# Kernel tuning notes

Hardware: AMD Instinct MI355X
Metric: run time of the kernel (lower is better)

## Reference

```python
import jax, jax.numpy as jnp
import numpy as np

DEPTH, HEADS, DH, BUCKET, NHASH = 4, 8, 64, 64, 4
DIM, VOCAB, BATCH, SEQ = 512, 50000, 2, 2048
LN_EPS = 1e-5
SELF_ATTN_VAL = -5e4  # TOKEN_SELF_ATTN_VALUE in reformer_pytorch


def layer_norm(x, s, b):
    mu = x.mean(-1, keepdims=True)
    var = ((x - mu) ** 2).mean(-1, keepdims=True)
    return (x - mu) / jnp.sqrt(var + LN_EPS) * s + b


def sincos(t, dh):
    # FixedPositionalEmbedding: emb = cat(sin, cos) of t x dh/2 angles
    inv = 1.0 / (10000.0 ** (jnp.arange(0, dh, 2, dtype=jnp.float32) / dh))
    ang = jnp.arange(t, dtype=jnp.float32)[:, None] * inv[None, :]
    return jnp.sin(ang), jnp.cos(ang)


def apply_rotary(qk, sin, cos):
    # qk: [B*H, T, DH]; sin/cos: [T, DH/2]; interleaved-pair rotary as in reformer_pytorch
    sin2 = jnp.repeat(sin, 2, axis=-1)[None]
    cos2 = jnp.repeat(cos, 2, axis=-1)[None]
    xr = qk.reshape(qk.shape[0], qk.shape[1], -1, 2)
    rot = jnp.stack((-xr[..., 1], xr[..., 0]), axis=-1).reshape(qk.shape)
    return qk * cos2 + rot * sin2


def lsh_attention(qk, v, rot):
    # qk, v: [B, T, dh] (B = batch*heads, shared-QK); rot: [dh, NHASH, n_buckets//2]
    B, T, dh = qk.shape
    nb = T // BUCKET
    rv = jnp.einsum('btf,fhi->bhti', qk, rot)           # [B, NHASH, T, nb/2]
    rv = jnp.concatenate([rv, -rv], axis=-1)
    buckets = jnp.argmax(rv, axis=-1)                    # [B, NHASH, T]
    buckets = (buckets + (jnp.arange(NHASH) * nb)[None, :, None]).reshape(B, NHASH * T)
    ticker = jnp.arange(NHASH * T) % T
    key = T * buckets + ticker[None, :]                  # unique sort keys
    sticker = jnp.argsort(key, axis=-1)                  # [B, NHASH*T]
    undo = jnp.argsort(sticker, axis=-1)
    st = sticker % T
    sqk = jnp.take_along_axis(qk, st[:, :, None], axis=1)
    sv = jnp.take_along_axis(v, st[:, :, None], axis=1)
    C = NHASH * nb                                       # num chunks, each BUCKET long
    bq_t = st.reshape(B, C, BUCKET)
    bq = sqk.reshape(B, C, BUCKET, dh)
    bv = sv.reshape(B, C, BUCKET, dh)
    bk = bq / jnp.maximum(jnp.linalg.norm(bq, axis=-1, keepdims=True), 1e-12)

    def look_one_back(a):
        return jnp.concatenate([a, jnp.roll(a, 1, axis=1)], axis=2)

    bk, bv, bkv_t = look_one_back(bk), look_one_back(bv), look_one_back(bq_t)
    dots = jnp.einsum('bcie,bcje->bcij', bq, bk) * (dh ** -0.5)
    dots = jnp.where(bq_t[:, :, :, None] == bkv_t[:, :, None, :], SELF_ATTN_VAL, dots)
    lse = jax.nn.logsumexp(dots, axis=-1, keepdims=True)
    p = jnp.exp(dots - lse)
    bo = jnp.einsum('bcij,bcje->bcie', p, bv)
    so = bo.reshape(B, NHASH * T, dh)
    slog = lse.reshape(B, NHASH * T)
    o = jnp.take_along_axis(so, undo[:, :, None], axis=1).reshape(B, NHASH, T, dh)
    lg = jnp.take_along_axis(slog, undo, axis=1).reshape(B, NHASH, T, 1)
    w = jnp.exp(lg - jax.nn.logsumexp(lg, axis=1, keepdims=True))
    return jnp.sum(o * w, axis=1)                        # [B, T, dh]


def attn_block(x, s, bln, Wqk, Wv, Wo, bo, rot, sin, cos):
    b, t, _ = x.shape
    xn = layer_norm(x, s, bln)
    qk = (xn @ Wqk).reshape(b, t, HEADS, DH).transpose(0, 2, 1, 3).reshape(b * HEADS, t, DH)
    v = (xn @ Wv).reshape(b, t, HEADS, DH).transpose(0, 2, 1, 3).reshape(b * HEADS, t, DH)
    qk = apply_rotary(qk, sin, cos)
    o = lsh_attention(qk, v, rot)
    o = o.reshape(b, HEADS, t, DH).transpose(0, 2, 1, 3).reshape(b, t, HEADS * DH)
    return o @ Wo + bo


def ff_block(x, s, b, W1, b1, W2, b2):
    xn = layer_norm(x, s, b)
    return jax.nn.gelu(xn @ W1 + b1, approximate=False) @ W2 + b2


def reference(x, token_emb, ln1_s, ln1_b, Wqk, Wv, Wo, bo, ln2_s, ln2_b, W1, b1, W2, b2, rotations, lnf_s, lnf_b, Wf1, bf1, Wout, bout):
    e = token_emb[x]                                     # [B, T, DIM]
    sin, cos = sincos(x.shape[1], DH)
    x1 = x2 = e                                          # reversible twin streams
    for i in range(DEPTH):
        x1 = x1 + attn_block(x2, ln1_s[i], ln1_b[i], Wqk[i], Wv[i], Wo[i], bo[i], rotations[i], sin, cos)
        x2 = x2 + ff_block(x1, ln2_s[i], ln2_b[i], W1[i], b1[i], W2[i], b2[i])
    h = layer_norm((x1 + x2) * 0.5, lnf_s, lnf_b)
    h = h.mean(axis=1)
    h = jax.nn.relu(h @ Wf1 + bf1)
    return h @ Wout + bout


def setup_inputs():
    key = jax.random.key(0)
    ks = jax.random.split(key, 10)
    nb = SEQ // BUCKET
    s = 0.02
    return {
        'x': jax.random.randint(ks[0], (BATCH, SEQ), 0, VOCAB),
        'token_emb': jax.random.normal(ks[1], (VOCAB, DIM), jnp.float32) * s,
        'ln1_s': jnp.ones((DEPTH, DIM), jnp.float32),
        'ln1_b': jnp.zeros((DEPTH, DIM), jnp.float32),
        'Wqk': jax.random.normal(ks[2], (DEPTH, DIM, HEADS * DH), jnp.float32) * s,
        'Wv': jax.random.normal(ks[3], (DEPTH, DIM, HEADS * DH), jnp.float32) * s,
        'Wo': jax.random.normal(ks[4], (DEPTH, HEADS * DH, DIM), jnp.float32) * s,
        'bo': jnp.zeros((DEPTH, DIM), jnp.float32),
        'ln2_s': jnp.ones((DEPTH, DIM), jnp.float32),
        'ln2_b': jnp.zeros((DEPTH, DIM), jnp.float32),
        'W1': jax.random.normal(ks[5], (DEPTH, DIM, 4 * DIM), jnp.float32) * s,
        'b1': jnp.zeros((DEPTH, 4 * DIM), jnp.float32),
        'W2': jax.random.normal(ks[6], (DEPTH, 4 * DIM, DIM), jnp.float32) * s,
        'b2': jnp.zeros((DEPTH, DIM), jnp.float32),
        'rotations': jax.random.normal(ks[7], (DEPTH, DH, NHASH, nb // 2), jnp.float32),
        'lnf_s': jnp.ones((DIM,), jnp.float32),
        'lnf_b': jnp.zeros((DIM,), jnp.float32),
        'Wf1': jax.random.normal(ks[8], (DIM, 256), jnp.float32) * s,
        'bf1': jnp.zeros((256,), jnp.float32),
        'Wout': jax.random.normal(ks[9], (256, 1), jnp.float32) * s,
        'bout': jnp.zeros((1,), jnp.float32),
    }
```

## Files before the change

### kernel.cpp

```cpp
#include <hip/hip_runtime.h>
#include <math.h>

#define TSEQ   2048
#define DIMM   512
#define NHEAD  8
#define DHD    64
#define BHD    16
#define NHASHK 4
#define CHUNKS 128
#define FFD    2048
#define NROWS  4096

#define OFF_WQK 0
#define OFF_WV  262144
#define OFF_WO  524288
#define OFF_W1  786432
#define OFF_W2  1835008
#define WT_TOT  2883584

typedef unsigned short u16;
typedef _Float16 f16;
typedef __attribute__((ext_vector_type(8))) _Float16 f16x8;
typedef __attribute__((ext_vector_type(4))) float f32x4;
typedef __attribute__((ext_vector_type(8))) unsigned short ushort8v;
typedef __attribute__((ext_vector_type(4))) unsigned short ushort4v;

__device__ inline u16 h16(float f) {
  union { f16 h; u16 u; } x;
  x.h = (f16)f;
  return x.u;
}
__device__ inline float f16f(u16 u) {
  union { u16 u; f16 h; } x;
  x.u = u;
  return (float)x.h;
}
__device__ inline f16x8 mk8f(unsigned a, unsigned b, unsigned c, unsigned d) {
  union { unsigned u[4]; f16x8 v; } x;
  x.u[0] = a; x.u[1] = b; x.u[2] = c; x.u[3] = d;
  return x.v;
}
__device__ inline float gelu_exact(float v) {
  return 0.5f * v * (1.0f + erff(v * 0.70710678118654752f));
}
__device__ inline int swz128(int row, int colbyte) {
  return row * 128 + (colbyte ^ ((row & 7) << 4));
}
#define VT(d, k) ((d) * 264 + (((d) & 32) ? 8 : 0) + ((k) << 1))

__global__ __launch_bounds__(128) void k_embed(const int* __restrict__ x, const float* __restrict__ emb,
                                               float* __restrict__ x1, float* __restrict__ x2) {
  int row = blockIdx.x;
  int tok = x[row];
  float4 v = ((const float4*)(emb + (size_t)tok * DIMM))[threadIdx.x];
  ((float4*)(x1 + (size_t)row * DIMM))[threadIdx.x] = v;
  ((float4*)(x2 + (size_t)row * DIMM))[threadIdx.x] = v;
}

__global__ __launch_bounds__(256) void k_sincos(float* __restrict__ sin_t, float* __restrict__ cos_t) {
  int idx = blockIdx.x * 256 + threadIdx.x;
  int t = idx >> 5, i = idx & 31;
  float inv = powf(10000.0f, -(float)(2 * i) / 64.0f);
  float ang = (float)t * inv;
  sin_t[idx] = sinf(ang);
  cos_t[idx] = cosf(ang);
}

__global__ __launch_bounds__(256) void k_layernorm(const float* __restrict__ x, const float* __restrict__ g,
                                                   const float* __restrict__ b, u16* __restrict__ dst) {
  int row = blockIdx.x, tid = threadIdx.x;
  const float* xr = x + (size_t)row * DIMM;
  float v0 = xr[tid], v1 = xr[tid + 256];
  int lane = tid & 63, w = tid >> 6;
  __shared__ float red[8];
  float s = v0 + v1;
#pragma unroll
  for (int o = 32; o; o >>= 1) s += __shfl_xor(s, o);
  if (lane == 0) red[w] = s;
  __syncthreads();
  float mu = (red[0] + red[1] + red[2] + red[3]) * (1.0f / DIMM);
  float d0 = v0 - mu, d1 = v1 - mu;
  float q = d0 * d0 + d1 * d1;
#pragma unroll
  for (int o = 32; o; o >>= 1) q += __shfl_xor(q, o);
  if (lane == 0) red[4 + w] = q;
  __syncthreads();
  float var = (red[4] + red[5] + red[6] + red[7]) * (1.0f / DIMM);
  float rstd = 1.0f / sqrtf(var + 1e-5f);
  size_t base = (size_t)row * DIMM;
  dst[base + tid] = h16(d0 * rstd * g[tid] + b[tid]);
  dst[base + tid + 256] = h16(d1 * rstd * g[tid + 256] + b[tid + 256]);
}

__global__ __launch_bounds__(256) void k_prep(const float* __restrict__ Wqk, const float* __restrict__ Wv,
                                              const float* __restrict__ Wo, const float* __restrict__ W1,
                                              const float* __restrict__ W2, const float* __restrict__ rot,
                                              u16* __restrict__ wt16, u16* __restrict__ rt16) {
  __shared__ float tile[32][33];
  const int L = blockIdx.x / 2820;
  const int idx = blockIdx.x - L * 2820;
  Wqk += (size_t)L * 262144;
  Wv  += (size_t)L * 262144;
  Wo  += (size_t)L * 262144;
  W1  += (size_t)L * 1048576;
  W2  += (size_t)L * 1048576;
  rot += (size_t)L * 4096;
  u16* wt = wt16 + (size_t)L * WT_TOT;
  u16* rt = rt16 + (size_t)L * 4096;
  const float* src;
  u16* dh;
  int K, N, k0, n0;
  if (idx < 768) {
    int w = idx >> 8, r = idx & 255;
    K = 512; N = 512; k0 = (r >> 4) << 5; n0 = (r & 15) << 5;
    src = (w == 0) ? Wqk : (w == 1) ? Wv : Wo;
    dh = wt + (size_t)w * 262144;
  } else if (idx < 1792) {
    int r = idx - 768;
    K = 512; N = 2048; k0 = (r >> 6) << 5; n0 = (r & 63) << 5;
    src = W1; dh = wt + OFF_W1;
  } else if (idx < 2816) {
    int r = idx - 1792;
    K = 2048; N = 512; k0 = (r >> 4) << 5; n0 = (r & 15) << 5;
    src = W2; dh = wt + OFF_W2;
  } else {
    int r = idx - 2816;
    K = 64; N = 64; k0 = (r >> 1) << 5; n0 = (r & 1) << 5;
    src = rot; dh = rt;
  }
  const int t = threadIdx.x;
  const int r = t >> 3, c4 = (t & 7) << 2;
  float4 v = *(const float4*)&src[(size_t)(k0 + r) * N + n0 + c4];
  tile[r][c4] = v.x; tile[r][c4 + 1] = v.y; tile[r][c4 + 2] = v.z; tile[r][c4 + 3] = v.w;
  __syncthreads();
  u16 hs[4];
#pragma unroll
  for (int i = 0; i < 4; ++i) hs[i] = h16(tile[c4 + i][r]);
  size_t o = (size_t)(n0 + r) * K + k0 + c4;
  *(ushort4v*)&dh[o] = (ushort4v){hs[0], hs[1], hs[2], hs[3]};
}

template <int BM, int STORE>
__global__ __launch_bounds__(256) void k_gemm16(
    const u16* __restrict__ A, const u16* __restrict__ Bt,
    const float* __restrict__ bias, float* __restrict__ out,
    u16* __restrict__ out16, u16* __restrict__ qk16, u16* __restrict__ v16,
    int K, int N,
    const float* __restrict__ sin_t, const float* __restrict__ cos_t,
    const u16* __restrict__ rt16, int* __restrict__ bucket) {
  constexpr int MF = BM / 32;
  constexpr int ACH = BM / 32;
  __shared__ __align__(16) char AsB[BM * 128];
  __shared__ __align__(16) char BsB[64 * 128];
  const int bm = blockIdx.x * BM, bn = blockIdx.y << 6;
  const int tid = threadIdx.x, lane = tid & 63, wid = tid >> 6;
  const int wm = (wid >> 1) * (BM / 2), wn = (wid & 1) << 5;
  const int l16 = lane & 15, g = lane >> 4;
  f32x4 acc[MF][2];
#pragma unroll
  for (int m = 0; m < MF; ++m) { acc[m][0] = (f32x4){0,0,0,0}; acc[m][1] = (f32x4){0,0,0,0}; }

  const int srow = tid >> 3;
  const int scolb = (tid & 7) << 4;
  const u16* ap = A + (size_t)(bm + srow) * K + ((tid & 7) << 3);
  const u16* bp = Bt + (size_t)(bn + srow) * K + ((tid & 7) << 3);

  ushort8v paA[ACH], pbA[2], paB[ACH], pbB[2];
#pragma unroll
  for (int i = 0; i < ACH; ++i) paA[i] = *(const ushort8v*)(ap + (size_t)(i << 5) * K);
#pragma unroll
  for (int i = 0; i < 2; ++i) pbA[i] = *(const ushort8v*)(bp + (size_t)(i << 5) * K);
#pragma unroll
  for (int i = 0; i < ACH; ++i) paB[i] = *(const ushort8v*)(ap + (size_t)(i << 5) * K + 64);
#pragma unroll
  for (int i = 0; i < 2; ++i) pbB[i] = *(const ushort8v*)(bp + (size_t)(i << 5) * K + 64);

  auto gstep = [&](ushort8v (&PA)[ACH], ushort8v (&PB)[2], int S) {
#pragma unroll
    for (int i = 0; i < ACH; ++i)
      *(ushort8v*)(AsB + swz128(srow + (i << 5), scolb)) = PA[i];
#pragma unroll
    for (int i = 0; i < 2; ++i)
      *(ushort8v*)(BsB + swz128(srow + (i << 5), scolb)) = PB[i];
    __syncthreads();
    const int kf = (S + 2) << 6;
    if (kf < K) {
#pragma unroll
      for (int i = 0; i < ACH; ++i) PA[i] = *(const ushort8v*)(ap + (size_t)(i << 5) * K + kf);
#pragma unroll
      for (int i = 0; i < 2; ++i) PB[i] = *(const ushort8v*)(bp + (size_t)(i << 5) * K + kf);
    }
    f16x8 af[MF][2], bfr[2][2];
#pragma unroll
    for (int m = 0; m < MF; ++m)
#pragma unroll
      for (int ks = 0; ks < 2; ++ks)
        af[m][ks] = *(const f16x8*)(AsB + swz128(wm + (m << 4) + l16, ((ks << 2) + g) << 4));
#pragma unroll
    for (int n = 0; n < 2; ++n)
#pragma unroll
      for (int ks = 0; ks < 2; ++ks)
        bfr[n][ks] = *(const f16x8*)(BsB + swz128(wn + (n << 4) + l16, ((ks << 2) + g) << 4));
#pragma unroll
    for (int m = 0; m < MF; ++m)
#pragma unroll
      for (int n = 0; n < 2; ++n)
#pragma unroll
        for (int ks = 0; ks < 2; ++ks)
          acc[m][n] = __builtin_amdgcn_mfma_f32_16x16x32_f16(af[m][ks], bfr[n][ks], acc[m][n], 0, 0, 0);
    __syncthreads();
  };

  const int nsteps = K >> 6;
  for (int s = 0; s < nsteps; s += 2) {
    gstep(paA, pbA, s);
    gstep(paB, pbB, s + 1);
  }

  const bool do_bucket = (STORE == 5) && (bn < 512);
  ushort8v prt0{}, prt1{};
  if (do_bucket) {
    int i0 = tid, i1 = tid + 256;
    prt0 = *(const ushort8v*)(rt16 + (i0 >> 3) * 64 + ((i0 & 7) << 3));
    prt1 = *(const ushort8v*)(rt16 + (i1 >> 3) * 64 + ((i1 & 7) << 3));
  }

#pragma unroll
  for (int m = 0; m < MF; ++m) {
#pragma unroll
    for (int n = 0; n < 2; ++n) {
      const int gn = bn + wn + (n << 4) + l16;
      float bv = 0.f;
      if (STORE == 1 || STORE == 4) bv = bias[gn];
#pragma unroll
      for (int r = 0; r < 4; ++r) {
        const int gm = bm + wm + (m << 4) + (g << 2) + r;
        float val = acc[m][n][r];
        if (STORE == 1) {
          out[(size_t)gm * N + gn] += val + bv;
        } else if (STORE == 4) {
          out16[(size_t)gm * N + gn] = h16(gelu_exact(val + bv));
        } else {
          const float pv = __shfl_xor(val, 1);
          const int bb = gm >> 11, tt = gm & (TSEQ - 1);
          if (gn < 512) {
            const int hh = gn >> 6, dd = gn & 63;
            const int ip = dd >> 1;
            float cz = cos_t[tt * 32 + ip], sz = sin_t[tt * 32 + ip];
            float o = (dd & 1) ? (val * cz + pv * sz) : (val * cz - pv * sz);
            u16 oh = h16(o);
            qk16[((size_t)((bb * NHEAD + hh) * TSEQ + tt)) * DHD + dd] = oh;
            *(u16*)(AsB + swz128(gm - bm, dd << 1)) = oh;
          } else {
            const int gnn = gn - 512;
            const int hh = gnn >> 6, dd = gnn & 63;
            v16[((size_t)((bb * NHEAD + hh) * TSEQ + tt)) * DHD + dd] = h16(val);
          }
        }
      }
    }
  }

  if (do_bucket) {
    {
      int i0 = tid, i1 = tid + 256;
      *(ushort8v*)(BsB + swz128(i0 >> 3, (i0 & 7) << 4)) = prt0;
      *(ushort8v*)(BsB + swz128(i1 >> 3, (i1 & 7) << 4)) = prt1;
    }
    __syncthreads();
    const int bwm = (wid >> 1) << 5;
    const int bwn = (wid & 1) << 5;
    f32x4 bacc[2][2];
#pragma unroll
    for (int m = 0; m < 2; ++m) { bacc[m][0] = (f32x4){0,0,0,0}; bacc[m][1] = (f32x4){0,0,0,0}; }
#pragma unroll
    for (int ks = 0; ks < 2; ++ks) {
      f16x8 bfr[2];
#pragma unroll
      for (int n = 0; n < 2; ++n)
        bfr[n] = *(const f16x8*)(BsB + swz128(bwn + (n << 4) + l16, (ks << 6) + (g << 4)));
#pragma unroll
      for (int m = 0; m < 2; ++m) {
        f16x8 afr = *(const f16x8*)(AsB + swz128(bwm + (m << 4) + l16, (ks << 6) + (g << 4)));
#pragma unroll
        for (int n = 0; n < 2; ++n)
          bacc[m][n] = __builtin_amdgcn_mfma_f32_16x16x32_f16(afr, bfr[n], bacc[m][n], 0, 0, 0);
      }
    }
    const int bb = bm >> 11;
    const int hh = bn >> 6;
#pragma unroll
    for (int m = 0; m < 2; ++m)
#pragma unroll
      for (int n = 0; n < 2; ++n) {
        const int hcol = (bwn >> 4) + n;
#pragma unroll
        for (int r = 0; r < 4; ++r) {
          float v = bacc[m][n][r];
          float best = v; int bi = l16;
          if (-v > best) { best = -v; bi = 16 + l16; }
#pragma unroll
          for (int o = 1; o < 16; o <<= 1) {
            float ob = __shfl_xor(best, o);
            int obi = __shfl_xor(bi, o);
            if (ob > best || (ob == best && obi < bi)) { best = ob; bi = obi; }
          }
          if (l16 == 0) {
            int t = (bm & (TSEQ - 1)) + bwm + (m << 4) + (g << 2) + r;
            bucket[((size_t)((bb * NHEAD + hh) * NHASHK) + hcol) * TSEQ + t] = bi;
          }
        }
      }
  }
}

__global__ __launch_bounds__(256) void k_sort(const int* __restrict__ bucket, int* __restrict__ st) {
  __shared__ int hist[256][33];
  __shared__ int chunk[8][32];
  __shared__ int bbase[32];
  const int seg = blockIdx.x;
  const int tid = threadIdx.x;
  const int* bk = bucket + (size_t)seg * TSEQ;
  int4 u0 = *(const int4*)(bk + tid * 8);
  int4 u1 = *(const int4*)(bk + tid * 8 + 4);
  int myb[8] = {u0.x, u0.y, u0.z, u0.w, u1.x, u1.y, u1.z, u1.w};
#pragma unroll
  for (int j = 0; j < 33; ++j) hist[tid][j] = 0;
  __syncthreads();
#pragma unroll
  for (int i = 0; i < 8; ++i) hist[tid][myb[i]]++;
  __syncthreads();
  const int b = tid & 31, c = tid >> 5;
  int ssum = 0;
  for (int g2 = c * 32; g2 < c * 32 + 32; ++g2) ssum += hist[g2][b];
  chunk[c][b] = ssum;
  __syncthreads();
  if (tid < 32) {
    int run = 0;
    for (int cc = 0; cc < 8; ++cc) { int v = chunk[cc][tid]; chunk[cc][tid] = run; run += v; }
    bbase[tid] = run;
  }
  __syncthreads();
  if (tid == 0) {
    int s = 0;
    for (int j = 0; j < 32; ++j) { int v = bbase[j]; bbase[j] = s; s += v; }
  }
  __syncthreads();
  int run = chunk[c][b];
  for (int g2 = c * 32; g2 < c * 32 + 32; ++g2) { int v = hist[g2][b]; hist[g2][b] = run; run += v; }
  __syncthreads();
  int* dst = st + (size_t)seg * TSEQ;
#pragma unroll
  for (int i = 0; i < 8; ++i) {
    int bb2 = myb[i];
    int p = bbase[bb2] + hist[tid][bb2];
    hist[tid][bb2]++;
    dst[p] = tid * 8 + i;
  }
}

__global__ __launch_bounds__(256) void k_attn(const u16* __restrict__ qk16,
                                              const u16* __restrict__ v16,
                                              const int* __restrict__ st,
                                              u16* __restrict__ o4h, float* __restrict__ lg) {
  __shared__ __align__(16) char Kb[128 * 128];
  __shared__ __align__(16) char Vb[64 * 264 + 16];
  __shared__ float inv_norm[128];
  __shared__ int tids[128];
  __shared__ float pn[256];
  const int blk = blockIdx.x;
  const int c = blk & (CHUNKS - 1), bh = blk >> 7;
  const int h = c >> 5;
  const int tid = threadIdx.x, lane = tid & 63, wid = tid >> 6;
  const int l16 = lane & 15, g = lane >> 4;

  if (tid < 128) {
    int cc = (tid < 64) ? c : ((c + CHUNKS - 1) & (CHUNKS - 1));
    tids[tid] = st[bh * (NHASHK * TSEQ) + cc * 64 + (tid & 63)];
  }
  __syncthreads();
  {
    const int r = tid >> 1, hf = tid & 1;
    const u16* qsrc = qk16 + ((size_t)bh * TSEQ + tids[r]) * 64 + hf * 32;
    const u16* vsrc = v16 + ((size_t)bh * TSEQ + tids[r]) * 64 + hf * 32;
    float ss = 0.f;
#pragma unroll
    for (int i = 0; i < 4; ++i) {
      ushort8v u = *(const ushort8v*)(qsrc + i * 8);
      *(ushort8v*)(Kb + swz128(r, hf * 64 + i * 16)) = u;
#pragma unroll
      for (int j = 0; j < 8; ++j) { float f = f16f(u[j]); ss += f * f; }
      ushort8v vv8 = *(const ushort8v*)(vsrc + i * 8);
#pragma unroll
      for (int j = 0; j < 8; ++j)
        *(u16*)(Vb + VT(hf * 32 + i * 8 + j, r)) = vv8[j];
    }
    pn[tid] = ss;
  }
  __syncthreads();
  if (tid < 128) {
    float s2 = pn[2 * tid] + pn[2 * tid + 1];
    inv_norm[tid] = 1.0f / fmaxf(sqrtf(s2), 1e-12f);
  }
  __syncthreads();

  const int qrow = (wid << 4) + l16;
  const int tq = tids[qrow];
  const size_t obase = (size_t)(bh * NHASHK + h) * TSEQ + tq;

  f32x4 accs[8];
#pragma unroll
  for (int i = 0; i < 8; ++i) accs[i] = (f32x4){0, 0, 0, 0};
#pragma unroll
  for (int s = 0; s < 2; ++s) {
    f16x8 qf = *(const f16x8*)(Kb + swz128(qrow, ((s << 2) + g) << 4));
#pragma unroll
    for (int mf = 0; mf < 8; ++mf) {
      f16x8 afr = *(const f16x8*)(Kb + swz128(mf * 16 + l16, ((s << 2) + g) << 4));
      accs[mf] = __builtin_amdgcn_mfma_f32_16x16x32_f16(afr, qf, accs[mf], 0, 0, 0);
    }
  }
  float pv[8][4];
  float mx = -3e38f;
#pragma unroll
  for (int mf = 0; mf < 8; ++mf) {
    float4 invn = *(const float4*)&inv_norm[mf * 16 + g * 4];
    int4 tk = *(const int4*)&tids[mf * 16 + g * 4];
    float inva[4] = {invn.x, invn.y, invn.z, invn.w};
    int tka[4] = {tk.x, tk.y, tk.z, tk.w};
#pragma unroll
    for (int r = 0; r < 4; ++r) {
      float d = accs[mf][r] * inva[r] * 0.125f;
      if (tka[r] == tq) d = -5e4f;
      pv[mf][r] = d;
      mx = fmaxf(mx, d);
    }
  }
  mx = fmaxf(mx, __shfl_xor(mx, 16));
  mx = fmaxf(mx, __shfl_xor(mx, 32));
  float sum = 0.f;
#pragma unroll
  for (int mf = 0; mf < 8; ++mf)
#pragma unroll
    for (int r = 0; r < 4; ++r) {
      float e = __expf(pv[mf][r] - mx);
      pv[mf][r] = e;
      sum += e;
    }
  sum += __shfl_xor(sum, 16);
  sum += __shfl_xor(sum, 32);
  float lse = __logf(sum) + mx;
  float rs = 1.0f / sum;
  if (g == 0) lg[obase] = lse;
  unsigned P2[8][2];
#pragma unroll
  for (int mf = 0; mf < 8; ++mf)
#pragma unroll
    for (int m = 0; m < 2; ++m) {
      float p0 = pv[mf][2 * m] * rs, p1 = pv[mf][2 * m + 1] * rs;
      P2[mf][m] = (unsigned)h16(p0) | ((unsigned)h16(p1) << 16);
    }
  f32x4 acco[4];
#pragma unroll
  for (int i = 0; i < 4; ++i) acco[i] = (f32x4){0, 0, 0, 0};
#pragma unroll
  for (int s = 0; s < 4; ++s) {
    unsigned bw[4];
#pragma unroll
    for (int w = 0; w < 4; ++w) {
      int srl = l16 + (((2 * g + (w >> 1)) & 3) << 4);
      unsigned a0 = __shfl(P2[2 * s][w & 1], srl);
      unsigned a1 = __shfl(P2[2 * s + 1][w & 1], srl);
      bw[w] = (g >> 1) ? a1 : a0;
    }
    f16x8 pb = mk8f(bw[0], bw[1], bw[2], bw[3]);
    const int k0 = s * 32 + g * 8;
#pragma unroll
    for (int mf = 0; mf < 4; ++mf) {
      const int dcol = mf * 16 + l16;
      uint2 v0 = *(const uint2*)(Vb + VT(dcol, k0));
      uint2 v1 = *(const uint2*)(Vb + VT(dcol, k0 + 4));
      f16x8 vf = mk8f(v0.x, v0.y, v1.x, v1.y);
      acco[mf] = __builtin_amdgcn_mfma_f32_16x16x32_f16(vf, pb, acco[mf], 0, 0, 0);
    }
  }
#pragma unroll
  for (int mf = 0; mf < 4; ++mf) {
    ushort4v o4s = {h16(acco[mf][0]), h16(acco[mf][1]), h16(acco[mf][2]), h16(acco[mf][3])};
    *(ushort4v*)&o4h[obase * 64 + mf * 16 + g * 4] = o4s;
  }
}

__global__ __launch_bounds__(256) void k_combine(const u16* __restrict__ o4h, const float* __restrict__ lg,
                                                 u16* __restrict__ ctx16) {
  int tok = blockIdx.x * 4 + (threadIdx.x >> 6);
  int dd = threadIdx.x & 63;
  int bh = tok >> 11, t = tok & (TSEQ - 1);
  size_t base = (size_t)bh * NHASHK * TSEQ + t;
  float l0 = lg[base], l1 = lg[base + TSEQ], l2 = lg[base + 2 * TSEQ], l3 = lg[base + 3 * TSEQ];
  float m = fmaxf(fmaxf(l0, l1), fmaxf(l2, l3));
  float e0 = expf(l0 - m), e1 = expf(l1 - m), e2 = expf(l2 - m), e3 = expf(l3 - m);
  float inv = 1.0f / (e0 + e1 + e2 + e3);
  float o = (e0 * f16f(o4h[base * 64 + dd]) + e1 * f16f(o4h[(base + TSEQ) * 64 + dd]) +
             e2 * f16f(o4h[(base + 2 * TSEQ) * 64 + dd]) + e3 * f16f(o4h[(base + 3 * TSEQ) * 64 + dd])) * inv;
  int b = bh >> 3, hh = bh & 7;
  ctx16[((size_t)(b * TSEQ + t)) * DIMM + hh * DHD + dd] = h16(o);
}

__global__ __launch_bounds__(256) void k_colmean1(const float* __restrict__ x1, const float* __restrict__ x2,
                                                  float* __restrict__ part) {
  const int blk = blockIdx.x;
  const int bb = blk >> 8, ch = blk & 255;
  const int tid = threadIdx.x, lane = tid & 63, w = tid >> 6;
  __shared__ float red[8];
  float a0 = 0.f, a1 = 0.f;
  for (int i = 0; i < 8; ++i) {
    int row = bb * TSEQ + ch * 8 + i;
    size_t base = (size_t)row * DIMM;
    float v0 = 0.5f * (x1[base + tid] + x2[base + tid]);
    float v1 = 0.5f * (x1[base + tid + 256] + x2[base + tid + 256]);
    float s = v0 + v1;
#pragma unroll
    for (int o = 32; o; o >>= 1) s += __shfl_xor(s, o);
    if (lane == 0) red[w] = s;
    __syncthreads();
    float mu = (red[0] + red[1] + red[2] + red[3]) * (1.0f / DIMM);
    float d0 = v0 - mu, d1 = v1 - mu;
    float q = d0 * d0 + d1 * d1;
#pragma unroll
    for (int o = 32; o; o >>= 1) q += __shfl_xor(q, o);
    if (lane == 0) red[4 + w] = q;
    __syncthreads();
    float var = (red[4] + red[5] + red[6] + red[7]) * (1.0f / DIMM);
    float rstd = 1.0f / sqrtf(var + 1e-5f);
    a0 += d0 * rstd;
    a1 += d1 * rstd;
    __syncthreads();
  }
  part[(size_t)blk * DIMM + tid] = a0;
  part[(size_t)blk * DIMM + tid + 256] = a1;
}

__global__ __launch_bounds__(256) void k_colmean2(const float* __restrict__ part,
                                                  const float* __restrict__ g, const float* __restrict__ b,
                                                  float* __restrict__ hm) {
  int gidx = blockIdx.x * 256 + threadIdx.x;
  int oid = gidx >> 3, sub = gidx & 7;
  int bb = oid >> 9, d = oid & 511;
  float s = 0.f;
  for (int c = sub; c < 256; c += 8) s += part[((size_t)(bb * 256 + c)) * DIMM + d];
  s += __shfl_xor(s, 1);
  s += __shfl_xor(s, 2);
  s += __shfl_xor(s, 4);
  if (sub == 0) hm[oid] = s * (1.0f / TSEQ) * g[d] + b[d];
}

__global__ __launch_bounds__(256) void k_head1(const float* __restrict__ hm, const float* __restrict__ Wf1,
                                               float* __restrict__ r1p) {
  int b = blockIdx.x & 1, kc = blockIdx.x >> 1;
  int j = threadIdx.x;
  float acc = 0;
  for (int k = kc * 64; k < kc * 64 + 64; ++k) acc += hm[b * DIMM + k] * Wf1[k * 256 + j];
  r1p[(size_t)(kc * 2 + b) * 256 + j] = acc;
}

__global__ __launch_bounds__(256) void k_head2(const float* __restrict__ r1p, const float* __restrict__ bf1,
                                               const float* __restrict__ Wout, const float* __restrict__ bout,
                                               float* __restrict__ outp) {
  int b = blockIdx.x;
  int tid = threadIdx.x, lane = tid & 63, w = tid >> 6;
  float s = 0.f;
#pragma unroll
  for (int kc = 0; kc < 8; ++kc) s += r1p[(size_t)(kc * 2 + b) * 256 + tid];
  float v = fmaxf(s + bf1[tid], 0.0f) * Wout[tid];
#pragma unroll
  for (int o = 32; o; o >>= 1) v += __shfl_xor(v, o);
  __shared__ float red[4];
  if (lane == 0) red[w] = v;
  __syncthreads();
  if (tid == 0) outp[b] = red[0] + red[1] + red[2] + red[3] + bout[0];
}

extern "C" void kernel_launch(void* const* d_in, const int* in_sizes, int n_in,
                              void* d_out, int out_size, void* d_ws, size_t ws_size,
                              hipStream_t stream) {
  const int*   x         = (const int*)d_in[0];
  const float* token_emb = (const float*)d_in[1];
  const float* ln1_s     = (const float*)d_in[2];
  const float* ln1_b     = (const float*)d_in[3];
  const float* Wqk       = (const float*)d_in[4];
  const float* Wv        = (const float*)d_in[5];
  const float* Wo        = (const float*)d_in[6];
  const float* bo        = (const float*)d_in[7];
  const float* ln2_s     = (const float*)d_in[8];
  const float* ln2_b     = (const float*)d_in[9];
  const float* W1        = (const float*)d_in[10];
  const float* b1        = (const float*)d_in[11];
  const float* W2        = (const float*)d_in[12];
  const float* b2        = (const float*)d_in[13];
  const float* rotations = (const float*)d_in[14];
  const float* lnf_s     = (const float*)d_in[15];
  const float* lnf_b     = (const float*)d_in[16];
  const float* Wf1       = (const float*)d_in[17];
  const float* bf1       = (const float*)d_in[18];
  const float* Wout      = (const float*)d_in[19];
  const float* bout      = (const float*)d_in[20];
  float* out = (float*)d_out;

  char* ws = (char*)d_ws;
  size_t off = 0;
  auto alloc = [&](size_t nbytes) {
    char* p = ws + off;
    off += (nbytes + 255) & ~(size_t)255;
    return p;
  };
  float*  x1     = (float*)alloc((size_t)NROWS * DIMM * 4);
  float*  x2     = (float*)alloc((size_t)NROWS * DIMM * 4);
  u16*    xn16   = (u16*)alloc((size_t)NROWS * DIMM * 2);
  u16*    qk16   = (u16*)alloc((size_t)BHD * TSEQ * DHD * 2);
  u16*    v16    = (u16*)alloc((size_t)BHD * TSEQ * DHD * 2);
  u16*    ffh16  = (u16*)alloc((size_t)NROWS * FFD * 2);
  u16*    o4h    = (u16*)alloc((size_t)BHD * NHASHK * TSEQ * DHD * 2);
  float*  lg     = (float*)alloc((size_t)BHD * NHASHK * TSEQ * 4);
  float*  sin_t  = (float*)alloc((size_t)TSEQ * 32 * 4);
  float*  cos_t  = (float*)alloc((size_t)TSEQ * 32 * 4);
  float*  part   = (float*)alloc((size_t)512 * DIMM * 4);
  float*  hm     = (float*)alloc(2 * DIMM * 4);
  float*  r1p    = (float*)alloc(16 * 256 * 4);
  int*    bucket = (int*)alloc((size_t)BHD * NHASHK * TSEQ * 4);
  int*    st     = (int*)alloc((size_t)BHD * NHASHK * TSEQ * 4);
  u16*    wt16   = (u16*)alloc((size_t)4 * WT_TOT * 2);
  u16*    rott16 = (u16*)alloc((size_t)4 * 64 * 64 * 2);
  u16*    ctx16  = xn16;

  k_embed<<<NROWS, 128, 0, stream>>>(x, token_emb, x1, x2);
  k_sincos<<<(TSEQ * 32) / 256, 256, 0, stream>>>(sin_t, cos_t);
  k_prep<<<4 * 2820, 256, 0, stream>>>(Wqk, Wv, Wo, W1, W2, rotations, wt16, rott16);

  for (int L = 0; L < 4; ++L) {
    u16* wt = wt16 + (size_t)L * WT_TOT;
    u16* rt = rott16 + (size_t)L * 4096;

    k_layernorm<<<NROWS, 256, 0, stream>>>(x2, ln1_s + L * DIMM, ln1_b + L * DIMM, xn16);
    k_gemm16<64, 5><<<dim3(64, 16), 256, 0, stream>>>(
        xn16, wt + OFF_WQK, nullptr, nullptr, nullptr, qk16, v16, 512, 1024, sin_t, cos_t, rt, bucket);
    k_sort<<<BHD * NHASHK, 256, 0, stream>>>(bucket, st);
    k_attn<<<BHD * CHUNKS, 256, 0, stream>>>(qk16, v16, st, o4h, lg);
    k_combine<<<(BHD * TSEQ) / 4, 256, 0, stream>>>(o4h, lg, ctx16);
    k_gemm16<64, 1><<<dim3(64, 8), 256, 0, stream>>>(
        ctx16, wt + OFF_WO, bo + L * DIMM, x1, nullptr, nullptr, nullptr, 512, 512, nullptr, nullptr, nullptr, nullptr);
    k_layernorm<<<NROWS, 256, 0, stream>>>(x1, ln2_s + L * DIMM, ln2_b + L * DIMM, xn16);
    k_gemm16<64, 4><<<dim3(64, 32), 256, 0, stream>>>(
        xn16, wt + OFF_W1, b1 + L * FFD, nullptr, ffh16, nullptr, nullptr, 512, 2048, nullptr, nullptr, nullptr, nullptr);
    k_gemm16<64, 1><<<dim3(64, 8), 256, 0, stream>>>(
        ffh16, wt + OFF_W2, b2 + L * DIMM, x2, nullptr, nullptr, nullptr, 2048, 512, nullptr, nullptr, nullptr, nullptr);
  }

  k_colmean1<<<512, 256, 0, stream>>>(x1, x2, part);
  k_colmean2<<<32, 256, 0, stream>>>(part, lnf_s, lnf_b, hm);
  k_head1<<<16, 256, 0, stream>>>(hm, Wf1, r1p);
  k_head2<<<2, 256, 0, stream>>>(r1p, bf1, Wout, bout, out);
}
```

Measured before the change: 501.7 us.

## Fuse hash-round combine into Wo GEMM and widen W1 GEMM tile

```diff
diff --git a/kernel.cpp b/kernel.cpp
--- a/kernel.cpp
+++ b/kernel.cpp
@@ -140,8 +140,8 @@
   *(ushort4v*)&dh[o] = (ushort4v){hs[0], hs[1], hs[2], hs[3]};
 }
 
-template <int BM, int STORE>
-__global__ __launch_bounds__(256) void k_gemm16(
+template <int BM, int BN, int STORE>
+__global__ __launch_bounds__(256, 4) void k_gemm16(
     const u16* __restrict__ A, const u16* __restrict__ Bt,
     const float* __restrict__ bias, float* __restrict__ out,
     u16* __restrict__ out16, u16* __restrict__ qk16, u16* __restrict__ v16,
@@ -149,38 +149,42 @@
     const float* __restrict__ sin_t, const float* __restrict__ cos_t,
     const u16* __restrict__ rt16, int* __restrict__ bucket) {
   constexpr int MF = BM / 32;
+  constexpr int NF = BN / 32;
   constexpr int ACH = BM / 32;
+  constexpr int BCH = BN / 32;
   __shared__ __align__(16) char AsB[BM * 128];
-  __shared__ __align__(16) char BsB[64 * 128];
-  const int bm = blockIdx.x * BM, bn = blockIdx.y << 6;
+  __shared__ __align__(16) char BsB[BN * 128];
+  const int bm = blockIdx.x * BM, bn = blockIdx.y * BN;
   const int tid = threadIdx.x, lane = tid & 63, wid = tid >> 6;
-  const int wm = (wid >> 1) * (BM / 2), wn = (wid & 1) << 5;
+  const int wm = (wid >> 1) * (BM / 2), wn = (wid & 1) * (BN / 2);
   const int l16 = lane & 15, g = lane >> 4;
-  f32x4 acc[MF][2];
-#pragma unroll
-  for (int m = 0; m < MF; ++m) { acc[m][0] = (f32x4){0,0,0,0}; acc[m][1] = (f32x4){0,0,0,0}; }
+  f32x4 acc[MF][NF];
+#pragma unroll
+  for (int m = 0; m < MF; ++m)
+#pragma unroll
+    for (int n = 0; n < NF; ++n) acc[m][n] = (f32x4){0.f, 0.f, 0.f, 0.f};
 
   const int srow = tid >> 3;
   const int scolb = (tid & 7) << 4;
   const u16* ap = A + (size_t)(bm + srow) * K + ((tid & 7) << 3);
   const u16* bp = Bt + (size_t)(bn + srow) * K + ((tid & 7) << 3);
 
-  ushort8v paA[ACH], pbA[2], paB[ACH], pbB[2];
+  ushort8v paA[ACH], pbA[BCH], paB[ACH], pbB[BCH];
 #pragma unroll
   for (int i = 0; i < ACH; ++i) paA[i] = *(const ushort8v*)(ap + (size_t)(i << 5) * K);
 #pragma unroll
-  for (int i = 0; i < 2; ++i) pbA[i] = *(const ushort8v*)(bp + (size_t)(i << 5) * K);
+  for (int i = 0; i < BCH; ++i) pbA[i] = *(const ushort8v*)(bp + (size_t)(i << 5) * K);
 #pragma unroll
   for (int i = 0; i < ACH; ++i) paB[i] = *(const ushort8v*)(ap + (size_t)(i << 5) * K + 64);
 #pragma unroll
-  for (int i = 0; i < 2; ++i) pbB[i] = *(const ushort8v*)(bp + (size_t)(i << 5) * K + 64);
-
-  auto gstep = [&](ushort8v (&PA)[ACH], ushort8v (&PB)[2], int S) {
+  for (int i = 0; i < BCH; ++i) pbB[i] = *(const ushort8v*)(bp + (size_t)(i << 5) * K + 64);
+
+  auto gstep = [&](ushort8v (&PA)[ACH], ushort8v (&PB)[BCH], int S) {
 #pragma unroll
     for (int i = 0; i < ACH; ++i)
       *(ushort8v*)(AsB + swz128(srow + (i << 5), scolb)) = PA[i];
 #pragma unroll
-    for (int i = 0; i < 2; ++i)
+    for (int i = 0; i < BCH; ++i)
       *(ushort8v*)(BsB + swz128(srow + (i << 5), scolb)) = PB[i];
     __syncthreads();
     const int kf = (S + 2) << 6;
@@ -188,26 +192,23 @@
 #pragma unroll
       for (int i = 0; i < ACH; ++i) PA[i] = *(const ushort8v*)(ap + (size_t)(i << 5) * K + kf);
 #pragma unroll
-      for (int i = 0; i < 2; ++i) PB[i] = *(const ushort8v*)(bp + (size_t)(i << 5) * K + kf);
-    }
-    f16x8 af[MF][2], bfr[2][2];
-#pragma unroll
-    for (int m = 0; m < MF; ++m)
-#pragma unroll
-      for (int ks = 0; ks < 2; ++ks)
-        af[m][ks] = *(const f16x8*)(AsB + swz128(wm + (m << 4) + l16, ((ks << 2) + g) << 4));
-#pragma unroll
-    for (int n = 0; n < 2; ++n)
-#pragma unroll
-      for (int ks = 0; ks < 2; ++ks)
-        bfr[n][ks] = *(const f16x8*)(BsB + swz128(wn + (n << 4) + l16, ((ks << 2) + g) << 4));
-#pragma unroll
-    for (int m = 0; m < MF; ++m)
-#pragma unroll
-      for (int n = 0; n < 2; ++n)
-#pragma unroll
-        for (int ks = 0; ks < 2; ++ks)
-          acc[m][n] = __builtin_amdgcn_mfma_f32_16x16x32_f16(af[m][ks], bfr[n][ks], acc[m][n], 0, 0, 0);
+      for (int i = 0; i < BCH; ++i) PB[i] = *(const ushort8v*)(bp + (size_t)(i << 5) * K + kf);
+    }
+#pragma unroll
+    for (int ks = 0; ks < 2; ++ks) {
+      f16x8 af[MF], bfr[NF];
+#pragma unroll
+      for (int m = 0; m < MF; ++m)
+        af[m] = *(const f16x8*)(AsB + swz128(wm + (m << 4) + l16, ((ks << 2) + g) << 4));
+#pragma unroll
+      for (int n = 0; n < NF; ++n)
+        bfr[n] = *(const f16x8*)(BsB + swz128(wn + (n << 4) + l16, ((ks << 2) + g) << 4));
+#pragma unroll
+      for (int m = 0; m < MF; ++m)
+#pragma unroll
+        for (int n = 0; n < NF; ++n)
+          acc[m][n] = __builtin_amdgcn_mfma_f32_16x16x32_f16(af[m], bfr[n], acc[m][n], 0, 0, 0);
+    }
     __syncthreads();
   };
 
@@ -228,7 +229,7 @@
 #pragma unroll
   for (int m = 0; m < MF; ++m) {
 #pragma unroll
-    for (int n = 0; n < 2; ++n) {
+    for (int n = 0; n < NF; ++n) {
       const int gn = bn + wn + (n << 4) + l16;
       float bv = 0.f;
       if (STORE == 1 || STORE == 4) bv = bias[gn];
@@ -314,6 +315,100 @@
   }
 }
 
+__global__ __launch_bounds__(256, 2) void k_gemm_wo(
+    const u16* __restrict__ o4h, const float* __restrict__ lg,
+    const u16* __restrict__ Bt, const float* __restrict__ bias,
+    float* __restrict__ out) {
+  __shared__ __align__(16) char AsB[64 * 128];
+  __shared__ __align__(16) char BsB[64 * 128];
+  const int bm = blockIdx.x << 6, bn = blockIdx.y << 6;
+  const int tid = threadIdx.x, lane = tid & 63, wid = tid >> 6;
+  const int wm = (wid >> 1) << 5, wn = (wid & 1) << 5;
+  const int l16 = lane & 15, g = lane >> 4;
+  f32x4 acc[2][2];
+#pragma unroll
+  for (int m = 0; m < 2; ++m) { acc[m][0] = (f32x4){0,0,0,0}; acc[m][1] = (f32x4){0,0,0,0}; }
+
+  const int srow = tid >> 3, scolb = (tid & 7) << 4, dd0 = (tid & 7) << 3;
+  const int t0 = bm + srow, t1 = t0 + 32;
+  const int b0 = t0 >> 11, tt0 = t0 & (TSEQ - 1);
+  const int b1 = t1 >> 11, tt1 = t1 & (TSEQ - 1);
+  const u16* bp = Bt + (size_t)(bn + srow) * 512 + dd0;
+
+  ushort8v rA0[4], rA1[4], rB0[4], rB1[4], pbA[2], pbB[2];
+  auto fetch = [&](ushort8v (&R0)[4], ushort8v (&R1)[4], ushort8v (&PB)[2], int s) {
+#pragma unroll
+    for (int h = 0; h < 4; ++h) {
+      R0[h] = *(const ushort8v*)(o4h + (((size_t)((b0 * 8 + s) * 4 + h) * TSEQ + tt0) << 6) + dd0);
+      R1[h] = *(const ushort8v*)(o4h + (((size_t)((b1 * 8 + s) * 4 + h) * TSEQ + tt1) << 6) + dd0);
+    }
+#pragma unroll
+    for (int i = 0; i < 2; ++i) PB[i] = *(const ushort8v*)(bp + (size_t)(i << 5) * 512 + (s << 6));
+  };
+  fetch(rA0, rA1, pbA, 0);
+  fetch(rB0, rB1, pbB, 1);
+
+  auto combine = [&](ushort8v (&R)[4], int b, int tt, int s) -> ushort8v {
+    size_t base = (size_t)((b * 8 + s) * 4) * TSEQ + tt;
+    float l0 = lg[base], l1 = lg[base + TSEQ], l2 = lg[base + 2 * TSEQ], l3 = lg[base + 3 * TSEQ];
+    float m = fmaxf(fmaxf(l0, l1), fmaxf(l2, l3));
+    float e0 = __expf(l0 - m), e1 = __expf(l1 - m), e2 = __expf(l2 - m), e3 = __expf(l3 - m);
+    float inv = 1.0f / (e0 + e1 + e2 + e3);
+    e0 *= inv; e1 *= inv; e2 *= inv; e3 *= inv;
+    ushort8v o;
+#pragma unroll
+    for (int j = 0; j < 8; ++j)
+      o[j] = h16(e0 * f16f(R[0][j]) + e1 * f16f(R[1][j]) + e2 * f16f(R[2][j]) + e3 * f16f(R[3][j]));
+    return o;
+  };
+
+  auto gstep = [&](ushort8v (&R0)[4], ushort8v (&R1)[4], ushort8v (&PB)[2], int s) {
+    ushort8v a0 = combine(R0, b0, tt0, s);
+    ushort8v a1 = combine(R1, b1, tt1, s);
+    *(ushort8v*)(AsB + swz128(srow, scolb)) = a0;
+    *(ushort8v*)(AsB + swz128(srow + 32, scolb)) = a1;
+    *(ushort8v*)(BsB + swz128(srow, scolb)) = PB[0];
+    *(ushort8v*)(BsB + swz128(srow + 32, scolb)) = PB[1];
+    __syncthreads();
+    if (s + 2 < 8) fetch(R0, R1, PB, s + 2);
+#pragma unroll
+    for (int ks = 0; ks < 2; ++ks) {
+      f16x8 af[2], bfr[2];
+#pragma unroll
+      for (int m = 0; m < 2; ++m)
+        af[m] = *(const f16x8*)(AsB + swz128(wm + (m << 4) + l16, ((ks << 2) + g) << 4));
+#pragma unroll
+      for (int n = 0; n < 2; ++n)
+        bfr[n] = *(const f16x8*)(BsB + swz128(wn + (n << 4) + l16, ((ks << 2) + g) << 4));
+#pragma unroll
+      for (int m = 0; m < 2; ++m)
+#pragma unroll
+        for (int n = 0; n < 2; ++n)
+          acc[m][n] = __builtin_amdgcn_mfma_f32_16x16x32_f16(af[m], bfr[n], acc[m][n], 0, 0, 0);
+    }
+    __syncthreads();
+  };
+
+  for (int s = 0; s < 8; s += 2) {
+    gstep(rA0, rA1, pbA, s);
+    gstep(rB0, rB1, pbB, s + 1);
+  }
+
+#pragma unroll
+  for (int m = 0; m < 2; ++m) {
+#pragma unroll
+    for (int n = 0; n < 2; ++n) {
+      const int gn = bn + wn + (n << 4) + l16;
+      const float bv = bias[gn];
+#pragma unroll
+      for (int r = 0; r < 4; ++r) {
+        const int gm = bm + wm + (m << 4) + (g << 2) + r;
+        out[(size_t)gm * 512 + gn] += acc[m][n][r] + bv;
+      }
+    }
+  }
+}
+
 __global__ __launch_bounds__(256) void k_sort(const int* __restrict__ bucket, int* __restrict__ st) {
   __shared__ int hist[256][33];
   __shared__ int chunk[8][32];
@@ -489,22 +584,6 @@
     ushort4v o4s = {h16(acco[mf][0]), h16(acco[mf][1]), h16(acco[mf][2]), h16(acco[mf][3])};
     *(ushort4v*)&o4h[obase * 64 + mf * 16 + g * 4] = o4s;
   }
-}
-
-__global__ __launch_bounds__(256) void k_combine(const u16* __restrict__ o4h, const float* __restrict__ lg,
-                                                 u16* __restrict__ ctx16) {
-  int tok = blockIdx.x * 4 + (threadIdx.x >> 6);
-  int dd = threadIdx.x & 63;
-  int bh = tok >> 11, t = tok & (TSEQ - 1);
-  size_t base = (size_t)bh * NHASHK * TSEQ + t;
-  float l0 = lg[base], l1 = lg[base + TSEQ], l2 = lg[base + 2 * TSEQ], l3 = lg[base + 3 * TSEQ];
-  float m = fmaxf(fmaxf(l0, l1), fmaxf(l2, l3));
-  float e0 = expf(l0 - m), e1 = expf(l1 - m), e2 = expf(l2 - m), e3 = expf(l3 - m);
-  float inv = 1.0f / (e0 + e1 + e2 + e3);
-  float o = (e0 * f16f(o4h[base * 64 + dd]) + e1 * f16f(o4h[(base + TSEQ) * 64 + dd]) +
-             e2 * f16f(o4h[(base + 2 * TSEQ) * 64 + dd]) + e3 * f16f(o4h[(base + 3 * TSEQ) * 64 + dd])) * inv;
-  int b = bh >> 3, hh = bh & 7;
-  ctx16[((size_t)(b * TSEQ + t)) * DIMM + hh * DHD + dd] = h16(o);
 }
 
 __global__ __launch_bounds__(256) void k_colmean1(const float* __restrict__ x1, const float* __restrict__ x2,
@@ -631,7 +710,6 @@
   int*    st     = (int*)alloc((size_t)BHD * NHASHK * TSEQ * 4);
   u16*    wt16   = (u16*)alloc((size_t)4 * WT_TOT * 2);
   u16*    rott16 = (u16*)alloc((size_t)4 * 64 * 64 * 2);
-  u16*    ctx16  = xn16;
 
   k_embed<<<NROWS, 128, 0, stream>>>(x, token_emb, x1, x2);
   k_sincos<<<(TSEQ * 32) / 256, 256, 0, stream>>>(sin_t, cos_t);
@@ -642,17 +720,15 @@
     u16* rt = rott16 + (size_t)L * 4096;
 
     k_layernorm<<<NROWS, 256, 0, stream>>>(x2, ln1_s + L * DIMM, ln1_b + L * DIMM, xn16);
-    k_gemm16<64, 5><<<dim3(64, 16), 256, 0, stream>>>(
+    k_gemm16<64, 64, 5><<<dim3(64, 16), 256, 0, stream>>>(
         xn16, wt + OFF_WQK, nullptr, nullptr, nullptr, qk16, v16, 512, 1024, sin_t, cos_t, rt, bucket);
     k_sort<<<BHD * NHASHK, 256, 0, stream>>>(bucket, st);
     k_attn<<<BHD * CHUNKS, 256, 0, stream>>>(qk16, v16, st, o4h, lg);
-    k_combine<<<(BHD * TSEQ) / 4, 256, 0, stream>>>(o4h, lg, ctx16);
-    k_gemm16<64, 1><<<dim3(64, 8), 256, 0, stream>>>(
-        ctx16, wt + OFF_WO, bo + L * DIMM, x1, nullptr, nullptr, nullptr, 512, 512, nullptr, nullptr, nullptr, nullptr);
+    k_gemm_wo<<<dim3(64, 8), 256, 0, stream>>>(o4h, lg, wt + OFF_WO, bo + L * DIMM, x1);
     k_layernorm<<<NROWS, 256, 0, stream>>>(x1, ln2_s + L * DIMM, ln2_b + L * DIMM, xn16);
-    k_gemm16<64, 4><<<dim3(64, 32), 256, 0, stream>>>(
+    k_gemm16<64, 128, 4><<<dim3(64, 16), 256, 0, stream>>>(
         xn16, wt + OFF_W1, b1 + L * FFD, nullptr, ffh16, nullptr, nullptr, 512, 2048, nullptr, nullptr, nullptr, nullptr);
-    k_gemm16<64, 1><<<dim3(64, 8), 256, 0, stream>>>(
+    k_gemm16<64, 64, 1><<<dim3(64, 8), 256, 0, stream>>>(
         ffh16, wt + OFF_W2, b2 + L * DIMM, x2, nullptr, nullptr, nullptr, 2048, 512, nullptr, nullptr, nullptr, nullptr);
   }
 
```

Measured after the change: 561.3 us. 1.12x slower.
